# Kernel tuning notes

Hardware: AMD Instinct MI355X
Metric: run time of the kernel (lower is better)

The kernel has to match this reference:

```python
import jax, jax.numpy as jnp
import numpy as np

KT = 1.0

def l2norm(x, eps=1e-12):
    # torch F.normalize(p=2): x / max(||x||, eps)
    n = jnp.sqrt(jnp.sum(x * x, axis=-1, keepdims=True))
    return x / jnp.maximum(n, eps)

def setup_inputs() -> dict:
    key = jax.random.key(0)
    k1, k2, k3 = jax.random.split(key, 3)
    B, T, key_dim, e_dim, n_e = 16, 1024, 256, 256, 512
    key_soft = jax.random.normal(k1, (B, T, key_dim), dtype=jnp.float32)
    # embedding tables init uniform(-1/n_e, 1/n_e) as in the torch module
    keys = jax.random.uniform(k2, (n_e, key_dim), minval=-1.0 / n_e, maxval=1.0 / n_e, dtype=jnp.float32)
    vparams = jax.random.uniform(k3, (n_e, e_dim), minval=-1.0 / n_e, maxval=1.0 / n_e, dtype=jnp.float32)
    return {"key_soft": key_soft, "keys": keys, "vparams": vparams}

def reference(key_soft, keys, vparams):
    # clustering_forward of VQClassifierNN
    ksn = l2norm(key_soft)                                  # [B,T,D]
    keys_norm = l2norm(keys)                                # [n_e,D]
    score_ksh = jnp.einsum('btd,nd->btn', ksn, keys_norm)   # [B,T,n_e]
    score_kss = jnp.einsum('btd,bsd->bts', ksn, ksn)        # [B,T,T]
    # softmax weighting over codebook (score_to_weight)
    w = jax.nn.softmax(score_ksh / KT, axis=-1)
    w = jnp.nan_to_num(w)
    vp_norm = l2norm(vparams)                               # [n_e,E]
    vparams_w = l2norm(jnp.einsum('btn,ne->bte', w, vp_norm))  # [B,T,E]
    score_vpss = jnp.einsum('bte,bse->bts', vparams_w, vparams_w)  # [B,T,T]
    score_vpsh = jnp.einsum('bte,ne->btn', vparams_w, vp_norm)     # [B,T,n_e]
    encoding_indices = jnp.argmax(score_ksh, axis=-1)       # [B,T] int
    vparams_hard = l2norm(vparams[encoding_indices])        # gather + normalize
    # straight-through: grads flow through vparams_w
    vparams_hard = vparams_w + jax.lax.stop_gradient(vparams_hard - vparams_w)
    return (encoding_indices, vparams_w, vparams_hard,
            score_vpss, score_vpsh, score_kss, score_ksh)
```

## Files before the change

kernel.cpp:

```cpp
#include <hip/hip_runtime.h>
#include <hip/hip_bf16.h>

#define BB 16
#define TT 1024
#define DD 256
#define NE 512
#define BT 16384

typedef unsigned short ushort_t;
typedef unsigned long long ull_t;
typedef __attribute__((ext_vector_type(8))) short bf16x8;
typedef __attribute__((ext_vector_type(4))) float f32x4;

#define AS_GLOBAL __attribute__((address_space(1)))
#define AS_SHARED __attribute__((address_space(3)))

static __device__ __forceinline__ ushort_t f2bf(float f) {
    union { float f; unsigned u; } x; x.f = f;
    unsigned r = x.u + 0x7fffu + ((x.u >> 16) & 1u);
    return (ushort_t)(r >> 16);
}

static __device__ __forceinline__ int xcd_swz(int bid, int grid) {
    const int cpx = grid >> 3;
    return (bid & 7) * cpx + (bid >> 3);
}

__global__ __launch_bounds__(256) void prep_all(const float* __restrict__ ks,
                                                const float* __restrict__ keys,
                                                const float* __restrict__ vparams,
                                                ushort_t* __restrict__ ksn_bf,
                                                ushort_t* __restrict__ keys_n_bf,
                                                float* __restrict__ vp_n,
                                                ushort_t* __restrict__ vp_n_bf,
                                                ushort_t* __restrict__ vpnT_bf) {
    const int bid = blockIdx.x;
    const int t = threadIdx.x;
    if (bid < 4096) {
        const int row  = bid * 4 + (t >> 6);
        const int lane = t & 63;
        const float4 v = *(const float4*)(ks + (long long)row * DD + lane * 4);
        float ss = v.x * v.x + v.y * v.y + v.z * v.z + v.w * v.w;
        #pragma unroll
        for (int off = 32; off > 0; off >>= 1) ss += __shfl_down(ss, off, 64);
        ss = __shfl(ss, 0, 64);
        const float inv = 1.0f / fmaxf(sqrtf(ss), 1e-12f);
        ull_t p =
              (ull_t)f2bf(v.x * inv)
            | ((ull_t)f2bf(v.y * inv) << 16)
            | ((ull_t)f2bf(v.z * inv) << 32)
            | ((ull_t)f2bf(v.w * inv) << 48);
        *(ull_t*)(ksn_bf + (long long)row * DD + lane * 4) = p;
    } else {
        const int b2 = bid - 4096;
        const bool is_keys = (b2 < NE);
        const int rr = is_keys ? b2 : b2 - NE;
        const float* src = (is_keys ? keys : vparams) + (long long)rr * DD;
        const float v = src[t];
        float ss = v * v;
        #pragma unroll
        for (int off = 32; off > 0; off >>= 1) ss += __shfl_down(ss, off, 64);
        __shared__ float partial[4];
        const int wave = t >> 6, lane = t & 63;
        if (lane == 0) partial[wave] = ss;
        __syncthreads();
        __shared__ float s_inv;
        if (t == 0) {
            float tot = partial[0] + partial[1] + partial[2] + partial[3];
            s_inv = 1.0f / fmaxf(sqrtf(tot), 1e-12f);
        }
        __syncthreads();
        const float r = v * s_inv;
        const ushort_t b = f2bf(r);
        if (is_keys) {
            keys_n_bf[(long long)rr * DD + t] = b;
        } else {
            vp_n[(long long)rr * DD + t] = r;
            vp_n_bf[(long long)rr * DD + t] = b;
            vpnT_bf[(long long)t * NE + rr] = b;
        }
    }
}

__global__ __launch_bounds__(256) void mega_gemm(const ushort_t* __restrict__ Ab,
                                                 float* __restrict__ Cb,
                                                 const ushort_t* __restrict__ Af,
                                                 const ushort_t* __restrict__ Bf,
                                                 float* __restrict__ Cf) {
    const int swz = xcd_swz(blockIdx.x, 1088);
    const ushort_t *A, *Bm;
    float* C;
    int bm, bn, ldc;
    bool sym;
    if (swz < 576) {
        const int z = swz / 36;
        int tt = swz - z * 36;
        int i = 0;
        while (tt >= 8 - i) { tt -= 8 - i; ++i; }
        const int j = i + tt;
        A  = Ab + (long long)z * TT * DD;
        Bm = A;
        C  = Cb + (long long)z * TT * TT;
        bm = i * 128; bn = j * 128; ldc = TT;
        sym = (i != j);
    } else {
        const int f = swz - 576;
        A = Af; Bm = Bf; C = Cf;
        bm = (f >> 2) * 128; bn = (f & 3) * 128; ldc = NE;
        sym = false;
    }

    __shared__ ushort_t As[2][128 * 32];
    __shared__ ushort_t Bs[2][128 * 32];

    const int tid = threadIdx.x;
    const int wv = tid >> 6;
    const int ln = tid & 63;
    const int srow   = ln >> 2;
    const int schunk = (ln & 3) * 8;
    const int wm = (wv >> 1) * 64;
    const int wn = (wv & 1) * 64;
    const int fr = ln & 15;
    const int fq = (ln >> 4) * 8;

    f32x4 acc[4][4] = {};

#define MG_STAGE(buf, kk)                                                          \
    {                                                                              \
        _Pragma("unroll")                                                          \
        for (int s = 0; s < 2; ++s) {                                              \
            const int ra = wv * 32 + s * 16;                                       \
            const ushort_t* ga = A + (long long)(bm + ra + srow) * DD + (kk) + schunk; \
            __builtin_amdgcn_global_load_lds((const AS_GLOBAL void*)ga,            \
                (AS_SHARED void*)&As[buf][ra * 32], 16, 0, 0);                     \
            const ushort_t* gb = Bm + (long long)(bn + ra + srow) * DD + (kk) + schunk; \
            __builtin_amdgcn_global_load_lds((const AS_GLOBAL void*)gb,            \
                (AS_SHARED void*)&Bs[buf][ra * 32], 16, 0, 0);                     \
        }                                                                          \
    }

#define MG_COMPUTE(buf)                                                            \
    {                                                                              \
        bf16x8 af[4], bfr[4];                                                      \
        _Pragma("unroll")                                                          \
        for (int i = 0; i < 4; ++i)                                                \
            af[i] = *(const bf16x8*)&As[buf][(wm + i * 16 + fr) * 32 + fq];        \
        _Pragma("unroll")                                                          \
        for (int j = 0; j < 4; ++j)                                                \
            bfr[j] = *(const bf16x8*)&Bs[buf][(wn + j * 16 + fr) * 32 + fq];       \
        _Pragma("unroll")                                                          \
        for (int i = 0; i < 4; ++i)                                                \
            _Pragma("unroll")                                                      \
            for (int j = 0; j < 4; ++j)                                            \
                acc[i][j] = __builtin_amdgcn_mfma_f32_16x16x32_bf16(af[i], bfr[j], acc[i][j], 0, 0, 0); \
    }

    MG_STAGE(0, 0);
    __syncthreads();
    int cur = 0;
    #pragma unroll
    for (int k0 = 32; k0 < DD; k0 += 32) {
        MG_STAGE(cur ^ 1, k0);
        MG_COMPUTE(cur);
        __syncthreads();
        cur ^= 1;
    }
    MG_COMPUTE(cur);

    const int col  = ln & 15;
    const int qrow = (ln >> 4) * 4;
    #pragma unroll
    for (int i = 0; i < 4; ++i)
        #pragma unroll
        for (int j = 0; j < 4; ++j)
            #pragma unroll
            for (int r = 0; r < 4; ++r)
                C[(long long)(bm + wm + i * 16 + qrow + r) * ldc + bn + wn + j * 16 + col] = acc[i][j][r];

    if (sym) {
        #pragma unroll
        for (int i = 0; i < 4; ++i)
            #pragma unroll
            for (int j = 0; j < 4; ++j) {
                float4 v = make_float4(acc[i][j][0], acc[i][j][1], acc[i][j][2], acc[i][j][3]);
                *(float4*)&C[(long long)(bn + wn + j * 16 + col) * ldc + bm + wm + i * 16 + qrow] = v;
            }
    }
#undef MG_STAGE
#undef MG_COMPUTE
}

__global__ __launch_bounds__(256) void softmax_argmax(const float* __restrict__ S,
                                                      const float* __restrict__ ks_raw,
                                                      const float* __restrict__ keys_raw,
                                                      float* __restrict__ idx_out,
                                                      ushort_t* __restrict__ W) {
    const int row  = blockIdx.x * 4 + (threadIdx.x >> 6);
    const int lane = threadIdx.x & 63;
    const long long base = (long long)row * NE;

    const float4 va = *(const float4*)(S + base + lane * 4);
    const float4 vb = *(const float4*)(S + base + 256 + lane * 4);

    float m8 = fmaxf(fmaxf(fmaxf(va.x, va.y), fmaxf(va.z, va.w)),
                     fmaxf(fmaxf(vb.x, vb.y), fmaxf(vb.z, vb.w)));
    #pragma unroll
    for (int off = 32; off > 0; off >>= 1) m8 = fmaxf(m8, __shfl_xor(m8, off, 64));
    const float m = m8;

    const float thr = m - 0.02f;
    unsigned mask = (va.x >= thr ? 1u : 0u) | (va.y >= thr ? 2u : 0u)
                  | (va.z >= thr ? 4u : 0u) | (va.w >= thr ? 8u : 0u)
                  | (vb.x >= thr ? 16u : 0u) | (vb.y >= thr ? 32u : 0u)
                  | (vb.z >= thr ? 64u : 0u) | (vb.w >= thr ? 128u : 0u);
    ull_t bal = __ballot(mask != 0);

    const float4 af = *(const float4*)(ks_raw + (long long)row * DD + lane * 4);
    double best = -1e300; int besti = 0x7fffffff;
    while (bal) {
        const int src = (int)__builtin_ctzll(bal);
        bal &= bal - 1;
        unsigned sm = (unsigned)__shfl((int)mask, src, 64);
        while (sm) {
            const int slot = __builtin_ctz(sm);
            sm &= sm - 1;
            const int c = (slot < 4) ? (src * 4 + slot) : (256 + src * 4 + slot - 4);
            const float4 bf4 = *(const float4*)(keys_raw + (long long)c * DD + lane * 4);
            double dp = (double)af.x * (double)bf4.x + (double)af.y * (double)bf4.y
                      + (double)af.z * (double)bf4.z + (double)af.w * (double)bf4.w;
            double nb = (double)bf4.x * (double)bf4.x + (double)bf4.y * (double)bf4.y
                      + (double)bf4.z * (double)bf4.z + (double)bf4.w * (double)bf4.w;
            #pragma unroll
            for (int off = 32; off > 0; off >>= 1) {
                dp += __shfl_xor(dp, off, 64);
                nb += __shfl_xor(nb, off, 64);
            }
            const double d = dp / sqrt(nb);
            if (d > best || (d == best && c < besti)) { best = d; besti = c; }
        }
    }
    if (lane == 0) idx_out[row] = (float)besti;

    const float e0 = expf(va.x - m), e1 = expf(va.y - m), e2 = expf(va.z - m), e3 = expf(va.w - m);
    const float e4 = expf(vb.x - m), e5 = expf(vb.y - m), e6 = expf(vb.z - m), e7 = expf(vb.w - m);
    float ssum = ((e0 + e1) + (e2 + e3)) + ((e4 + e5) + (e6 + e7));
    #pragma unroll
    for (int off = 32; off > 0; off >>= 1) ssum += __shfl_xor(ssum, off, 64);
    const float inv = 1.0f / ssum;
    ull_t p0 = (ull_t)f2bf(e0 * inv) | ((ull_t)f2bf(e1 * inv) << 16)
             | ((ull_t)f2bf(e2 * inv) << 32) | ((ull_t)f2bf(e3 * inv) << 48);
    ull_t p1 = (ull_t)f2bf(e4 * inv) | ((ull_t)f2bf(e5 * inv) << 16)
             | ((ull_t)f2bf(e6 * inv) << 32) | ((ull_t)f2bf(e7 * inv) << 48);
    *(ull_t*)(W + base + lane * 4) = p0;
    *(ull_t*)(W + base + 256 + lane * 4) = p1;
}

__global__ __launch_bounds__(256) void gemm_vpw_norm(const ushort_t* __restrict__ Aw,
                                                     const ushort_t* __restrict__ BvT,
                                                     const float* __restrict__ idxf,
                                                     const float* __restrict__ vp_n,
                                                     float* __restrict__ vpw,
                                                     ushort_t* __restrict__ vpw_bf,
                                                     float* __restrict__ vph) {
    const int bm = xcd_swz(blockIdx.x, 512) * 32;

    __shared__ ushort_t As[2][32 * 32];
    __shared__ ushort_t Bs[2][256 * 32];

    const int tid = threadIdx.x;
    const int wv = tid >> 6;
    const int ln = tid & 63;
    const int srow   = ln >> 2;
    const int schunk = (ln & 3) * 8;
    const int wn = wv * 64;
    const int fr = ln & 15;
    const int fq = (ln >> 4) * 8;

    f32x4 acc[2][4] = {};

#define VW_STAGE(buf, kk)                                                          \
    {                                                                              \
        _Pragma("unroll")                                                          \
        for (int s = 0; s < 5; ++s) {                                              \
            const int g = wv * 5 + s;                                              \
            if (g < 16) {                                                          \
                const int rb = g * 16;                                             \
                const ushort_t* gb = BvT + (long long)(rb + srow) * NE + (kk) + schunk; \
                __builtin_amdgcn_global_load_lds((const AS_GLOBAL void*)gb,        \
                    (AS_SHARED void*)&Bs[buf][rb * 32], 16, 0, 0);                 \
            } else if (g < 18) {                                                   \
                const int ra = (g - 16) * 16;                                      \
                const ushort_t* ga = Aw + (long long)(bm + ra + srow) * NE + (kk) + schunk; \
                __builtin_amdgcn_global_load_lds((const AS_GLOBAL void*)ga,        \
                    (AS_SHARED void*)&As[buf][ra * 32], 16, 0, 0);                 \
            }                                                                      \
        }                                                                          \
    }

#define VW_COMPUTE(buf)                                                            \
    {                                                                              \
        bf16x8 af[2], bfr[4];                                                      \
        _Pragma("unroll")                                                          \
        for (int i = 0; i < 2; ++i)                                                \
            af[i] = *(const bf16x8*)&As[buf][(i * 16 + fr) * 32 + fq];             \
        _Pragma("unroll")                                                          \
        for (int j = 0; j < 4; ++j)                                                \
            bfr[j] = *(const bf16x8*)&Bs[buf][(wn + j * 16 + fr) * 32 + fq];       \
        _Pragma("unroll")                                                          \
        for (int i = 0; i < 2; ++i)                                                \
            _Pragma("unroll")                                                      \
            for (int j = 0; j < 4; ++j)                                            \
                acc[i][j] = __builtin_amdgcn_mfma_f32_16x16x32_bf16(af[i], bfr[j], acc[i][j], 0, 0, 0); \
    }

    VW_STAGE(0, 0);
    __syncthreads();
    int cur = 0;
    for (int k0 = 32; k0 < NE; k0 += 32) {
        VW_STAGE(cur ^ 1, k0);
        VW_COMPUTE(cur);
        __syncthreads();
        cur ^= 1;
    }
    VW_COMPUTE(cur);

    __shared__ float sq[32][4];
    __shared__ float inv_s[32];
    __shared__ int   sidx[32];
    const int qrow = (ln >> 4) * 4;
    #pragma unroll
    for (int i = 0; i < 2; ++i) {
        #pragma unroll
        for (int r = 0; r < 4; ++r) {
            float s = 0.0f;
            #pragma unroll
            for (int j = 0; j < 4; ++j) { const float a = acc[i][j][r]; s += a * a; }
            #pragma unroll
            for (int msk = 1; msk < 16; msk <<= 1) s += __shfl_xor(s, msk, 64);
            if ((ln & 15) == 0) sq[i * 16 + qrow + r][wv] = s;
        }
    }
    if (tid < 32) sidx[tid] = (int)idxf[bm + tid];
    __syncthreads();
    if (tid < 32) {
        const float tot = sq[tid][0] + sq[tid][1] + sq[tid][2] + sq[tid][3];
        inv_s[tid] = 1.0f / fmaxf(sqrtf(tot), 1e-12f);
    }
    __syncthreads();

    const int col = ln & 15;
    #pragma unroll
    for (int i = 0; i < 2; ++i)
        #pragma unroll
        for (int r = 0; r < 4; ++r) {
            const int row = i * 16 + qrow + r;
            const float iv = inv_s[row];
            #pragma unroll
            for (int j = 0; j < 4; ++j) {
                const float v = acc[i][j][r] * iv;
                const long long o = (long long)(bm + row) * DD + wn + j * 16 + col;
                vpw[o] = v;
                vpw_bf[o] = f2bf(v);
            }
        }

    #pragma unroll 4
    for (int k = 0; k < 32; ++k) {
        const int grow = bm + k;
        vph[(long long)grow * DD + tid] = vp_n[(long long)sidx[k] * DD + tid];
    }
#undef VW_STAGE
#undef VW_COMPUTE
}

extern "C" void kernel_launch(void* const* d_in, const int* in_sizes, int n_in,
                              void* d_out, int out_size, void* d_ws, size_t ws_size,
                              hipStream_t stream) {
    const float* key_soft = (const float*)d_in[0];
    const float* keys     = (const float*)d_in[1];
    const float* vparams  = (const float*)d_in[2];
    float* out = (float*)d_out;

    const long long off0 = 0;
    const long long off1 = off0 + BT;
    const long long off2 = off1 + (long long)BT * DD;
    const long long off3 = off2 + (long long)BT * DD;
    const long long off4 = off3 + (long long)BB * TT * TT;
    const long long off5 = off4 + (long long)BT * NE;
    const long long off6 = off5 + (long long)BB * TT * TT;

    float* o_idx  = out + off0;
    float* o_vpw  = out + off1;
    float* o_vph  = out + off2;
    float* o_vpss = out + off3;
    float* o_vpsh = out + off4;
    float* o_kss  = out + off5;
    float* o_ksh  = out + off6;

    float*    vp_n      = (float*)d_ws;
    ushort_t* vp_n_bf   = (ushort_t*)(vp_n + (long long)NE * DD);
    ushort_t* vpnT_bf   = vp_n_bf + (long long)NE * DD;
    ushort_t* vpw_bf    = vpnT_bf + (long long)DD * NE;
    ushort_t* keys_n_bf = vpw_bf + (long long)BT * DD;

    ushort_t* ksn_bf = (ushort_t*)o_vpsh;
    ushort_t* w_bf   = (ushort_t*)(o_vpss + (long long)BT * DD);

    prep_all<<<4096 + 2 * NE, 256, 0, stream>>>(
        key_soft, keys, vparams, ksn_bf, keys_n_bf, vp_n, vp_n_bf, vpnT_bf);

    mega_gemm<<<576 + 512, 256, 0, stream>>>(
        ksn_bf, o_kss, ksn_bf, keys_n_bf, o_ksh);

    softmax_argmax<<<BT / 4, 256, 0, stream>>>(o_ksh, key_soft, keys, o_idx, w_bf);

    gemm_vpw_norm<<<512, 256, 0, stream>>>(
        w_bf, vpnT_bf, o_idx, vp_n, o_vpw, vpw_bf, o_vph);

    mega_gemm<<<576 + 512, 256, 0, stream>>>(
        vpw_bf, o_vpss, vpw_bf, vp_n_bf, o_vpsh);
}
```

Measured before the change: 312.2 us.

## Fuse softmax/argmax into weighted vparams GEMM keeping weights in LDS

Merges the softmax+argmax kernel with the GEMM that forms vparams_w. Each block computes softmax weights for its 32 rows and stores them in swizzled shared memory, which then serves directly as the A operand. This removes the global write and read of the bf16 weight matrix and one kernel launch. In exchange, the softmax phase runs with far fewer blocks, and the block uses more LDS, which may lower occupancy.

```diff
diff --git a/kernel.cpp b/kernel.cpp
--- a/kernel.cpp
+++ b/kernel.cpp
@@ -190,119 +190,120 @@
 #undef MG_COMPUTE
 }
 
-__global__ __launch_bounds__(256) void softmax_argmax(const float* __restrict__ S,
-                                                      const float* __restrict__ ks_raw,
-                                                      const float* __restrict__ keys_raw,
-                                                      float* __restrict__ idx_out,
-                                                      ushort_t* __restrict__ W) {
-    const int row  = blockIdx.x * 4 + (threadIdx.x >> 6);
-    const int lane = threadIdx.x & 63;
-    const long long base = (long long)row * NE;
-
-    const float4 va = *(const float4*)(S + base + lane * 4);
-    const float4 vb = *(const float4*)(S + base + 256 + lane * 4);
-
-    float m8 = fmaxf(fmaxf(fmaxf(va.x, va.y), fmaxf(va.z, va.w)),
-                     fmaxf(fmaxf(vb.x, vb.y), fmaxf(vb.z, vb.w)));
-    #pragma unroll
-    for (int off = 32; off > 0; off >>= 1) m8 = fmaxf(m8, __shfl_xor(m8, off, 64));
-    const float m = m8;
-
-    const float thr = m - 0.02f;
-    unsigned mask = (va.x >= thr ? 1u : 0u) | (va.y >= thr ? 2u : 0u)
-                  | (va.z >= thr ? 4u : 0u) | (va.w >= thr ? 8u : 0u)
-                  | (vb.x >= thr ? 16u : 0u) | (vb.y >= thr ? 32u : 0u)
-                  | (vb.z >= thr ? 64u : 0u) | (vb.w >= thr ? 128u : 0u);
-    ull_t bal = __ballot(mask != 0);
-
-    const float4 af = *(const float4*)(ks_raw + (long long)row * DD + lane * 4);
-    double best = -1e300; int besti = 0x7fffffff;
-    while (bal) {
-        const int src = (int)__builtin_ctzll(bal);
-        bal &= bal - 1;
-        unsigned sm = (unsigned)__shfl((int)mask, src, 64);
-        while (sm) {
-            const int slot = __builtin_ctz(sm);
-            sm &= sm - 1;
-            const int c = (slot < 4) ? (src * 4 + slot) : (256 + src * 4 + slot - 4);
-            const float4 bf4 = *(const float4*)(keys_raw + (long long)c * DD + lane * 4);
-            double dp = (double)af.x * (double)bf4.x + (double)af.y * (double)bf4.y
-                      + (double)af.z * (double)bf4.z + (double)af.w * (double)bf4.w;
-            double nb = (double)bf4.x * (double)bf4.x + (double)bf4.y * (double)bf4.y
-                      + (double)bf4.z * (double)bf4.z + (double)bf4.w * (double)bf4.w;
-            #pragma unroll
-            for (int off = 32; off > 0; off >>= 1) {
-                dp += __shfl_xor(dp, off, 64);
-                nb += __shfl_xor(nb, off, 64);
+__global__ __launch_bounds__(256) void softmax_vpw(const float* __restrict__ S,
+                                                   const float* __restrict__ ks_raw,
+                                                   const float* __restrict__ keys_raw,
+                                                   const ushort_t* __restrict__ BvT,
+                                                   const float* __restrict__ vp_n,
+                                                   float* __restrict__ idx_out,
+                                                   float* __restrict__ vpw,
+                                                   ushort_t* __restrict__ vpw_bf,
+                                                   float* __restrict__ vph) {
+    const int bm = xcd_swz(blockIdx.x, 512) * 32;
+
+    __shared__ ushort_t Wl[32 * 512];
+    __shared__ ushort_t Bs[2][256 * 32];
+    __shared__ float sq[32][4];
+    __shared__ float qinv[32];
+    __shared__ int   sidx[32];
+
+    const int tid  = threadIdx.x;
+    const int wv   = tid >> 6;
+    const int lane = tid & 63;
+
+    for (int rr = wv; rr < 32; rr += 4) {
+        const int row = bm + rr;
+        const long long base = (long long)row * NE;
+        const float4 va = *(const float4*)(S + base + lane * 4);
+        const float4 vb = *(const float4*)(S + base + 256 + lane * 4);
+
+        float m8 = fmaxf(fmaxf(fmaxf(va.x, va.y), fmaxf(va.z, va.w)),
+                         fmaxf(fmaxf(vb.x, vb.y), fmaxf(vb.z, vb.w)));
+        #pragma unroll
+        for (int off = 32; off > 0; off >>= 1) m8 = fmaxf(m8, __shfl_xor(m8, off, 64));
+        const float m = m8;
+
+        const float thr = m - 0.02f;
+        unsigned mask = (va.x >= thr ? 1u : 0u) | (va.y >= thr ? 2u : 0u)
+                      | (va.z >= thr ? 4u : 0u) | (va.w >= thr ? 8u : 0u)
+                      | (vb.x >= thr ? 16u : 0u) | (vb.y >= thr ? 32u : 0u)
+                      | (vb.z >= thr ? 64u : 0u) | (vb.w >= thr ? 128u : 0u);
+        ull_t bal = __ballot(mask != 0);
+
+        const float4 af4 = *(const float4*)(ks_raw + (long long)row * DD + lane * 4);
+        double best = -1e300; int besti = 0x7fffffff;
+        while (bal) {
+            const int src = (int)__builtin_ctzll(bal);
+            bal &= bal - 1;
+            unsigned sm = (unsigned)__shfl((int)mask, src, 64);
+            while (sm) {
+                const int slot = __builtin_ctz(sm);
+                sm &= sm - 1;
+                const int c = (slot < 4) ? (src * 4 + slot) : (256 + src * 4 + slot - 4);
+                const float4 bf4 = *(const float4*)(keys_raw + (long long)c * DD + lane * 4);
+                double dp = (double)af4.x * (double)bf4.x + (double)af4.y * (double)bf4.y
+                          + (double)af4.z * (double)bf4.z + (double)af4.w * (double)bf4.w;
+                double nb = (double)bf4.x * (double)bf4.x + (double)bf4.y * (double)bf4.y
+                          + (double)bf4.z * (double)bf4.z + (double)bf4.w * (double)bf4.w;
+                #pragma unroll
+                for (int off = 32; off > 0; off >>= 1) {
+                    dp += __shfl_xor(dp, off, 64);
+                    nb += __shfl_xor(nb, off, 64);
+                }
+                const double d = dp / sqrt(nb);
+                if (d > best || (d == best && c < besti)) { best = d; besti = c; }
             }
-            const double d = dp / sqrt(nb);
-            if (d > best || (d == best && c < besti)) { best = d; besti = c; }
-        }
-    }
-    if (lane == 0) idx_out[row] = (float)besti;
-
-    const float e0 = expf(va.x - m), e1 = expf(va.y - m), e2 = expf(va.z - m), e3 = expf(va.w - m);
-    const float e4 = expf(vb.x - m), e5 = expf(vb.y - m), e6 = expf(vb.z - m), e7 = expf(vb.w - m);
-    float ssum = ((e0 + e1) + (e2 + e3)) + ((e4 + e5) + (e6 + e7));
-    #pragma unroll
-    for (int off = 32; off > 0; off >>= 1) ssum += __shfl_xor(ssum, off, 64);
-    const float inv = 1.0f / ssum;
-    ull_t p0 = (ull_t)f2bf(e0 * inv) | ((ull_t)f2bf(e1 * inv) << 16)
-             | ((ull_t)f2bf(e2 * inv) << 32) | ((ull_t)f2bf(e3 * inv) << 48);
-    ull_t p1 = (ull_t)f2bf(e4 * inv) | ((ull_t)f2bf(e5 * inv) << 16)
-             | ((ull_t)f2bf(e6 * inv) << 32) | ((ull_t)f2bf(e7 * inv) << 48);
-    *(ull_t*)(W + base + lane * 4) = p0;
-    *(ull_t*)(W + base + 256 + lane * 4) = p1;
-}
-
-__global__ __launch_bounds__(256) void gemm_vpw_norm(const ushort_t* __restrict__ Aw,
-                                                     const ushort_t* __restrict__ BvT,
-                                                     const float* __restrict__ idxf,
-                                                     const float* __restrict__ vp_n,
-                                                     float* __restrict__ vpw,
-                                                     ushort_t* __restrict__ vpw_bf,
-                                                     float* __restrict__ vph) {
-    const int bm = xcd_swz(blockIdx.x, 512) * 32;
-
-    __shared__ ushort_t As[2][32 * 32];
-    __shared__ ushort_t Bs[2][256 * 32];
-
-    const int tid = threadIdx.x;
-    const int wv = tid >> 6;
-    const int ln = tid & 63;
-    const int srow   = ln >> 2;
-    const int schunk = (ln & 3) * 8;
+        }
+        if (lane == 0) { idx_out[row] = (float)besti; sidx[rr] = besti; }
+
+        const float e0 = expf(va.x - m), e1 = expf(va.y - m), e2 = expf(va.z - m), e3 = expf(va.w - m);
+        const float e4 = expf(vb.x - m), e5 = expf(vb.y - m), e6 = expf(vb.z - m), e7 = expf(vb.w - m);
+        float ssum = ((e0 + e1) + (e2 + e3)) + ((e4 + e5) + (e6 + e7));
+        #pragma unroll
+        for (int off = 32; off > 0; off >>= 1) ssum += __shfl_xor(ssum, off, 64);
+        const float inv = 1.0f / ssum;
+        ull_t p0 = (ull_t)f2bf(e0 * inv) | ((ull_t)f2bf(e1 * inv) << 16)
+                 | ((ull_t)f2bf(e2 * inv) << 32) | ((ull_t)f2bf(e3 * inv) << 48);
+        ull_t p1 = (ull_t)f2bf(e4 * inv) | ((ull_t)f2bf(e5 * inv) << 16)
+                 | ((ull_t)f2bf(e6 * inv) << 32) | ((ull_t)f2bf(e7 * inv) << 48);
+        {
+            char* rowb = (char*)&Wl[rr * 512];
+            const int c0 = lane * 4;
+            *(ull_t*)(rowb + ((((c0 >> 3) ^ (rr & 7)) << 4) | ((c0 & 7) * 2))) = p0;
+            const int c1 = 256 + lane * 4;
+            *(ull_t*)(rowb + ((((c1 >> 3) ^ (rr & 7)) << 4) | ((c1 & 7) * 2))) = p1;
+        }
+    }
+    __syncthreads();
+
+    const int srow   = lane >> 2;
+    const int schunk = (lane & 3) * 8;
     const int wn = wv * 64;
-    const int fr = ln & 15;
-    const int fq = (ln >> 4) * 8;
+    const int fr = lane & 15;
+    const int fq = (lane >> 4) * 8;
 
     f32x4 acc[2][4] = {};
 
-#define VW_STAGE(buf, kk)                                                          \
+#define VB_STAGE(buf, kk)                                                          \
     {                                                                              \
         _Pragma("unroll")                                                          \
-        for (int s = 0; s < 5; ++s) {                                              \
-            const int g = wv * 5 + s;                                              \
-            if (g < 16) {                                                          \
-                const int rb = g * 16;                                             \
-                const ushort_t* gb = BvT + (long long)(rb + srow) * NE + (kk) + schunk; \
-                __builtin_amdgcn_global_load_lds((const AS_GLOBAL void*)gb,        \
-                    (AS_SHARED void*)&Bs[buf][rb * 32], 16, 0, 0);                 \
-            } else if (g < 18) {                                                   \
-                const int ra = (g - 16) * 16;                                      \
-                const ushort_t* ga = Aw + (long long)(bm + ra + srow) * NE + (kk) + schunk; \
-                __builtin_amdgcn_global_load_lds((const AS_GLOBAL void*)ga,        \
-                    (AS_SHARED void*)&As[buf][ra * 32], 16, 0, 0);                 \
-            }                                                                      \
+        for (int s = 0; s < 4; ++s) {                                              \
+            const int rb = (wv * 4 + s) * 16;                                      \
+            const ushort_t* gb = BvT + (long long)(rb + srow) * NE + (kk) + schunk; \
+            __builtin_amdgcn_global_load_lds((const AS_GLOBAL void*)gb,            \
+                (AS_SHARED void*)&Bs[buf][rb * 32], 16, 0, 0);                     \
         }                                                                          \
     }
 
-#define VW_COMPUTE(buf)                                                            \
+#define VB_COMPUTE(buf, kb)                                                        \
     {                                                                              \
-        bf16x8 af[2], bfr[4];                                                      \
-        _Pragma("unroll")                                                          \
-        for (int i = 0; i < 2; ++i)                                                \
-            af[i] = *(const bf16x8*)&As[buf][(i * 16 + fr) * 32 + fq];             \
+        bf16x8 afr[2], bfr[4];                                                     \
+        _Pragma("unroll")                                                          \
+        for (int i = 0; i < 2; ++i) {                                              \
+            const int R = i * 16 + fr;                                             \
+            afr[i] = *(const bf16x8*)((const char*)Wl +                            \
+                     (R * 1024 + (((((kb) + fq) >> 3) ^ (R & 7)) << 4)));          \
+        }                                                                          \
         _Pragma("unroll")                                                          \
         for (int j = 0; j < 4; ++j)                                                \
             bfr[j] = *(const bf16x8*)&Bs[buf][(wn + j * 16 + fr) * 32 + fq];       \
@@ -310,24 +311,21 @@
         for (int i = 0; i < 2; ++i)                                                \
             _Pragma("unroll")                                                      \
             for (int j = 0; j < 4; ++j)                                            \
-                acc[i][j] = __builtin_amdgcn_mfma_f32_16x16x32_bf16(af[i], bfr[j], acc[i][j], 0, 0, 0); \
-    }
-
-    VW_STAGE(0, 0);
+                acc[i][j] = __builtin_amdgcn_mfma_f32_16x16x32_bf16(afr[i], bfr[j], acc[i][j], 0, 0, 0); \
+    }
+
+    VB_STAGE(0, 0);
     __syncthreads();
     int cur = 0;
     for (int k0 = 32; k0 < NE; k0 += 32) {
-        VW_STAGE(cur ^ 1, k0);
-        VW_COMPUTE(cur);
+        VB_STAGE(cur ^ 1, k0);
+        VB_COMPUTE(cur, k0 - 32);
         __syncthreads();
         cur ^= 1;
     }
-    VW_COMPUTE(cur);
-
-    __shared__ float sq[32][4];
-    __shared__ float inv_s[32];
-    __shared__ int   sidx[32];
-    const int qrow = (ln >> 4) * 4;
+    VB_COMPUTE(cur, NE - 32);
+
+    const int qrow = (lane >> 4) * 4;
     #pragma unroll
     for (int i = 0; i < 2; ++i) {
         #pragma unroll
@@ -337,24 +335,23 @@
             for (int j = 0; j < 4; ++j) { const float a = acc[i][j][r]; s += a * a; }
             #pragma unroll
             for (int msk = 1; msk < 16; msk <<= 1) s += __shfl_xor(s, msk, 64);
-            if ((ln & 15) == 0) sq[i * 16 + qrow + r][wv] = s;
-        }
-    }
-    if (tid < 32) sidx[tid] = (int)idxf[bm + tid];
+            if ((lane & 15) == 0) sq[i * 16 + qrow + r][wv] = s;
+        }
+    }
     __syncthreads();
     if (tid < 32) {
         const float tot = sq[tid][0] + sq[tid][1] + sq[tid][2] + sq[tid][3];
-        inv_s[tid] = 1.0f / fmaxf(sqrtf(tot), 1e-12f);
+        qinv[tid] = 1.0f / fmaxf(sqrtf(tot), 1e-12f);
     }
     __syncthreads();
 
-    const int col = ln & 15;
+    const int col = lane & 15;
     #pragma unroll
     for (int i = 0; i < 2; ++i)
         #pragma unroll
         for (int r = 0; r < 4; ++r) {
             const int row = i * 16 + qrow + r;
-            const float iv = inv_s[row];
+            const float iv = qinv[row];
             #pragma unroll
             for (int j = 0; j < 4; ++j) {
                 const float v = acc[i][j][r] * iv;
@@ -365,12 +362,10 @@
         }
 
     #pragma unroll 4
-    for (int k = 0; k < 32; ++k) {
-        const int grow = bm + k;
-        vph[(long long)grow * DD + tid] = vp_n[(long long)sidx[k] * DD + tid];
-    }
-#undef VW_STAGE
-#undef VW_COMPUTE
+    for (int k = 0; k < 32; ++k)
+        vph[(long long)(bm + k) * DD + tid] = vp_n[(long long)sidx[k] * DD + tid];
+#undef VB_STAGE
+#undef VB_COMPUTE
 }
 
 extern "C" void kernel_launch(void* const* d_in, const int* in_sizes, int n_in,
@@ -404,7 +399,6 @@
     ushort_t* keys_n_bf = vpw_bf + (long long)BT * DD;
 
     ushort_t* ksn_bf = (ushort_t*)o_vpsh;
-    ushort_t* w_bf   = (ushort_t*)(o_vpss + (long long)BT * DD);
 
     prep_all<<<4096 + 2 * NE, 256, 0, stream>>>(
         key_soft, keys, vparams, ksn_bf, keys_n_bf, vp_n, vp_n_bf, vpnT_bf);
@@ -412,10 +406,8 @@
     mega_gemm<<<576 + 512, 256, 0, stream>>>(
         ksn_bf, o_kss, ksn_bf, keys_n_bf, o_ksh);
 
-    softmax_argmax<<<BT / 4, 256, 0, stream>>>(o_ksh, key_soft, keys, o_idx, w_bf);
-
-    gemm_vpw_norm<<<512, 256, 0, stream>>>(
-        w_bf, vpnT_bf, o_idx, vp_n, o_vpw, vpw_bf, o_vph);
+    softmax_vpw<<<512, 256, 0, stream>>>(
+        o_ksh, key_soft, keys, vpnT_bf, vp_n, o_idx, o_vpw, vpw_bf, o_vph);
 
     mega_gemm<<<576 + 512, 256, 0, stream>>>(
         vpw_bf, o_vpss, vpw_bf, vp_n_bf, o_vpsh);
```

Measured after the change: 321.4 us. 1.03x slower.
